# Kernel optimization log

Measured on AMD Instinct MI355X. Metric: run time of the kernel, lower is better.

## Reference

```python
import jax, jax.numpy as jnp
import numpy as np

N_NODES = 50000
N_EDGES = 800000
IN_DIM = 128
OUT_DIM = 128
N_HEADS = 4
HEAD_DIM = OUT_DIM // N_HEADS
EDGE_EMBED_DIM = 16
LN_EPS = 1e-5


def setup_inputs() -> dict:
    key = jax.random.key(0)
    ks = jax.random.split(key, 10)
    x = jax.random.normal(ks[0], (N_NODES, IN_DIM), dtype=jnp.float32)
    edge_index = jax.random.randint(ks[1], (2, N_EDGES), 0, N_NODES, dtype=jnp.int32)
    edge_type = jax.random.randint(ks[2], (N_EDGES,), 0, 3, dtype=jnp.int32)
    # parameters (xavier-ish scaling)
    W = jax.random.normal(ks[3], (OUT_DIM, IN_DIM), dtype=jnp.float32) * (1.0 / np.sqrt(IN_DIM))
    a_src = jax.random.normal(ks[4], (N_HEADS, HEAD_DIM), dtype=jnp.float32) * (1.0 / np.sqrt(HEAD_DIM))
    a_dst = jax.random.normal(ks[5], (N_HEADS, HEAD_DIM), dtype=jnp.float32) * (1.0 / np.sqrt(HEAD_DIM))
    a_edge = jax.random.normal(ks[6], (N_HEADS, EDGE_EMBED_DIM), dtype=jnp.float32) * (1.0 / np.sqrt(EDGE_EMBED_DIM))
    edge_embed = jax.random.normal(ks[7], (3, EDGE_EMBED_DIM), dtype=jnp.float32)
    ln_gamma = jnp.ones((OUT_DIM,), dtype=jnp.float32)
    ln_beta = jnp.zeros((OUT_DIM,), dtype=jnp.float32)
    return {"x": x, "edge_index": edge_index, "edge_type": edge_type,
            "W": W, "a_src": a_src, "a_dst": a_dst, "a_edge": a_edge,
            "edge_embed": edge_embed, "ln_gamma": ln_gamma, "ln_beta": ln_beta}


def reference(x, edge_index, edge_type, W, a_src, a_dst, a_edge, edge_embed, ln_gamma, ln_beta):
    N = x.shape[0]
    h = x @ W.T                                   # [N, out_dim]
    hh = h.reshape(N, N_HEADS, HEAD_DIM)          # [N, H, D]
    src, dst = edge_index[0], edge_index[1]       # [E]

    # per-node attention projections, then gather (avoids gathering full [E,H,D] twice)
    alpha_src = jnp.einsum('nhd,hd->nh', hh, a_src)   # [N, H]
    alpha_dst = jnp.einsum('nhd,hd->nh', hh, a_dst)   # [N, H]
    e_score = edge_embed[edge_type] @ a_edge.T        # [E, H]

    attn = alpha_src[src] + alpha_dst[dst] + e_score  # [E, H]
    attn = jax.nn.leaky_relu(attn, negative_slope=0.2)

    # segment softmax over incoming edges of each dst node
    attn_max = jax.ops.segment_max(attn, dst, num_segments=N)    # [N, H]
    attn_max = jnp.maximum(attn_max, -1e9)                       # match torch init fill
    attn_exp = jnp.exp(attn - attn_max[dst])                     # [E, H]
    attn_sum = jax.ops.segment_sum(attn_exp, dst, num_segments=N)
    attn_norm = attn_exp / (attn_sum[dst] + 1e-10)               # [E, H]

    # weighted scatter-aggregation (dropout is identity in eval)
    weighted = hh[src] * attn_norm[:, :, None]                   # [E, H, D]
    out = jax.ops.segment_sum(weighted, dst, num_segments=N)     # [N, H, D]
    out = out.reshape(N, OUT_DIM) + h                            # residual

    # LayerNorm over last dim
    mu = jnp.mean(out, axis=-1, keepdims=True)
    var = jnp.var(out, axis=-1, keepdims=True)
    out = (out - mu) * jax.lax.rsqrt(var + LN_EPS)
    return out * ln_gamma + ln_beta
```

## Files before the change

### kernel.cpp

```cpp
#include <hip/hip_runtime.h>

#define N_NODES 50000
#define N_EDGES 800000
#define IN_DIM 128
#define OUT_DIM 128
#define N_HEADS 4
#define HEAD_DIM 32
#define LN_EPS 1e-5f

#define WS_HB    0
#define WS_ASRC  3200000
#define WS_ADST  3400000
#define WS_ETAB  3600000
#define WS_DEG   3600016
#define WS_AVTAB 3650016
#define WS_OFFS  3650528
#define WS_PARTS 3700528
#define WS_EPACK 3700592
#define WS_RANK  4500608

#define SCAN_BLOCKS 49

typedef __bf16 bf16x8 __attribute__((ext_vector_type(8)));
typedef float  f32x4  __attribute__((ext_vector_type(4)));

__device__ __forceinline__ unsigned short f2bf(float f) {
    unsigned int u = __float_as_uint(f);
    u += 0x7FFF + ((u >> 16) & 1);
    return (unsigned short)(u >> 16);
}
#define BFLO(u) __uint_as_float((unsigned int)(u) << 16)
#define BFHI(u) __uint_as_float((unsigned int)(u) & 0xFFFF0000u)
#define LRELU(c) ((c) > 0.f ? (c) : 0.2f * (c))

__global__ __launch_bounds__(256) void zero_kernel(int4* __restrict__ p)
{
    int i = blockIdx.x * 256 + threadIdx.x;
    if (i < N_NODES / 4) p[i] = make_int4(0, 0, 0, 0);
}

__global__ __launch_bounds__(256) void count_prep_kernel(
    const int* __restrict__ dsts, int* __restrict__ deg, int* __restrict__ rank,
    const float* __restrict__ W, const float* __restrict__ a_src,
    const float* __restrict__ a_dst, const float* __restrict__ edge_embed,
    const float* __restrict__ a_edge, float* __restrict__ etab,
    unsigned short* __restrict__ avtab)
{
    int gid = blockIdx.x * 256 + threadIdx.x;
    if (gid < 12) {
        int t = gid >> 2, hh = gid & 3;
        float s = 0.f;
        for (int k = 0; k < 16; ++k) s += edge_embed[t * 16 + k] * a_edge[hh * 16 + k];
        etab[t * 4 + hh] = s;
    }
    if (gid < 1024) {
        int c8 = gid & 7, k = gid >> 3;
        int hh = c8 & 3;
        const float* av = (c8 < 4) ? a_src : a_dst;
        float s = 0.f;
        #pragma unroll 8
        for (int dd = 0; dd < 32; ++dd)
            s += W[(hh * 32 + dd) * 128 + k] * av[hh * 32 + dd];
        int kblk = k >> 5, g = (k & 31) >> 3, j = k & 7;
        avtab[((kblk * 64) + g * 16 + c8) * 8 + j] = f2bf(s);
    }
    if (gid < N_EDGES) rank[gid] = atomicAdd(&deg[dsts[gid]], 1);
}

__global__ __launch_bounds__(256) void gemm_mfma_kernel(
    const float* __restrict__ x, const float* __restrict__ W,
    const unsigned short* __restrict__ avtab,
    unsigned short* __restrict__ hb,
    float* __restrict__ alpha_src, float* __restrict__ alpha_dst)
{
    __shared__ bf16x8 wlds[2048];
    int tid = threadIdx.x;
    for (int f = tid; f < 2048; f += 256) {
        int ct = f >> 8, kb = (f >> 6) & 3, ln = f & 63;
        int d = ct * 16 + (ln & 15);
        int kbase = kb * 32 + ((ln >> 4) << 3);
        const float* wp = W + d * 128 + kbase;
        float4 w0 = *(const float4*)wp;
        float4 w1 = *(const float4*)(wp + 4);
        bf16x8 v;
        v[0] = (__bf16)w0.x; v[1] = (__bf16)w0.y; v[2] = (__bf16)w0.z; v[3] = (__bf16)w0.w;
        v[4] = (__bf16)w1.x; v[5] = (__bf16)w1.y; v[6] = (__bf16)w1.z; v[7] = (__bf16)w1.w;
        wlds[f] = v;
    }
    int lane = tid & 63, wid = tid >> 6;
    bf16x8 avf[4];
    const bf16x8* avp = (const bf16x8*)avtab;
    #pragma unroll
    for (int kb = 0; kb < 4; ++kb) avf[kb] = avp[kb * 64 + lane];
    __syncthreads();

    int r = lane & 15, g = lane >> 4;
    int tile = blockIdx.x * 4 + wid;
    if (tile >= N_NODES / 16) return;
    {
        const float* xp = x + ((size_t)tile * 16 + r) * 128 + g * 8;
        bf16x8 af[4];
        #pragma unroll
        for (int kb = 0; kb < 4; ++kb) {
            float4 x0 = *(const float4*)(xp + kb * 32);
            float4 x1 = *(const float4*)(xp + kb * 32 + 4);
            bf16x8 v;
            v[0] = (__bf16)x0.x; v[1] = (__bf16)x0.y; v[2] = (__bf16)x0.z; v[3] = (__bf16)x0.w;
            v[4] = (__bf16)x1.x; v[5] = (__bf16)x1.y; v[6] = (__bf16)x1.z; v[7] = (__bf16)x1.w;
            af[kb] = v;
        }
        f32x4 aacc = {0.f, 0.f, 0.f, 0.f};
        #pragma unroll
        for (int kb = 0; kb < 4; ++kb)
            aacc = __builtin_amdgcn_mfma_f32_16x16x32_bf16(af[kb], avf[kb], aacc, 0, 0, 0);

        int orow = tile * 16 + g * 4;
        #pragma unroll
        for (int ct = 0; ct < 8; ++ct) {
            f32x4 acc = {0.f, 0.f, 0.f, 0.f};
            #pragma unroll
            for (int kb = 0; kb < 4; ++kb)
                acc = __builtin_amdgcn_mfma_f32_16x16x32_bf16(af[kb], wlds[(ct * 4 + kb) * 64 + lane], acc, 0, 0, 0);
            #pragma unroll
            for (int q = 0; q < 4; ++q)
                hb[(size_t)(orow + q) * 128 + ct * 16 + r] = f2bf(acc[q]);
        }
        if (r < 8) {
            float* ap = (r < 4) ? (alpha_src + (r & 3)) : (alpha_dst + (r & 3));
            #pragma unroll
            for (int q = 0; q < 4; ++q)
                ap[(size_t)(orow + q) * 4] = aacc[q];
        }
    }
}

__global__ __launch_bounds__(1024) void scan_part_kernel(
    const int* __restrict__ deg, int* __restrict__ offs, int* __restrict__ parts)
{
    __shared__ int wsum[16];
    int i = blockIdx.x * 1024 + threadIdx.x;
    int lane = threadIdx.x & 63;
    int wid  = threadIdx.x >> 6;
    int v = (i < N_NODES) ? deg[i] : 0;
    int xinc = v;
    #pragma unroll
    for (int d = 1; d < 64; d <<= 1) {
        int y = __shfl_up(xinc, d);
        if (lane >= d) xinc += y;
    }
    if (lane == 63) wsum[wid] = xinc;
    __syncthreads();
    if (wid == 0) {
        int sv = (lane < 16) ? wsum[lane] : 0;
        #pragma unroll
        for (int d = 1; d < 16; d <<= 1) {
            int y = __shfl_up(sv, d);
            if (lane >= d) sv += y;
        }
        if (lane < 16) wsum[lane] = sv;
    }
    __syncthreads();
    int woff = (wid > 0) ? wsum[wid - 1] : 0;
    if (i < N_NODES) offs[i] = woff + xinc - v;
    if (threadIdx.x == 0) parts[blockIdx.x] = wsum[15];
}

__global__ __launch_bounds__(1024) void scan_add_kernel(
    int* __restrict__ offs, const int* __restrict__ parts)
{
    __shared__ int pre_s;
    if (threadIdx.x < 64) {
        int v = ((int)threadIdx.x < (int)blockIdx.x) ? parts[threadIdx.x] : 0;
        #pragma unroll
        for (int off = 32; off >= 1; off >>= 1) v += __shfl_xor(v, off);
        if (threadIdx.x == 0) pre_s = v;
    }
    __syncthreads();
    int i = blockIdx.x * 1024 + threadIdx.x;
    if (i < N_NODES) offs[i] += pre_s;
}

__global__ void fill_kernel(const int* __restrict__ srcs, const int* __restrict__ dsts,
                            const int* __restrict__ etype, const int* __restrict__ rank,
                            const int* __restrict__ offs, unsigned int* __restrict__ epack)
{
    int e = blockIdx.x * 256 + threadIdx.x;
    if (e < N_EDGES) {
        int d = dsts[e];
        int p = offs[d] + rank[e];
        epack[p] = (unsigned int)srcs[e] | ((unsigned int)etype[e] << 16);
    }
}

__global__ __launch_bounds__(256) void aggregate_kernel(
    const unsigned short* __restrict__ hb, const float* __restrict__ alpha_src,
    const float* __restrict__ alpha_dst, const float* __restrict__ etab,
    const unsigned int* __restrict__ epack, const int* __restrict__ offs,
    const float* __restrict__ gamma, const float* __restrict__ beta,
    float* __restrict__ out)
{
    int lane = threadIdx.x & 63;
    int wid  = threadIdx.x >> 6;
    int half = lane >> 5;
    int l5   = lane & 31;
    int n = blockIdx.x * 8 + wid * 2 + half;
    if (n >= N_NODES) return;

    int e0 = offs[n];
    int e1 = (n == N_NODES - 1) ? N_EDGES : offs[n + 1];
    int deg = e1 - e0;

    int g  = l5 >> 3;
    int sl = l5 & 7;
    int headL = sl >> 1;

    float ad_h = alpha_dst[(size_t)n * 4 + headL];
    float et0 = etab[0 * 4 + headL];
    float et1 = etab[1 * 4 + headL];
    float et2 = etab[2 * 4 + headL];

    float s = 0.f;
    float acc[16];
    #pragma unroll
    for (int k = 0; k < 16; ++k) acc[k] = 0.f;

    const unsigned int* ep = epack + e0;
    for (int j = g; j < deg; j += 4) {
        unsigned int p = ep[j];
        int si = p & 0xFFFF;
        int t  = p >> 16;
        float asv = alpha_src[(size_t)si * 4 + headL];
        const uint4* hp = (const uint4*)(hb + ((size_t)si << 7) + (sl << 4));
        uint4 hA = hp[0];
        uint4 hB = hp[1];
        float ev = (t == 0) ? et0 : ((t == 1) ? et1 : et2);
        float c = LRELU(asv + ad_h + ev);
        float w = __expf(c);
        s += w;
        acc[0]  += w * BFLO(hA.x); acc[1]  += w * BFHI(hA.x);
        acc[2]  += w * BFLO(hA.y); acc[3]  += w * BFHI(hA.y);
        acc[4]  += w * BFLO(hA.z); acc[5]  += w * BFHI(hA.z);
        acc[6]  += w * BFLO(hA.w); acc[7]  += w * BFHI(hA.w);
        acc[8]  += w * BFLO(hB.x); acc[9]  += w * BFHI(hB.x);
        acc[10] += w * BFLO(hB.y); acc[11] += w * BFHI(hB.y);
        acc[12] += w * BFLO(hB.z); acc[13] += w * BFHI(hB.z);
        acc[14] += w * BFLO(hB.w); acc[15] += w * BFHI(hB.w);
    }

    #pragma unroll
    for (int k = 0; k < 16; ++k) {
        acc[k] += __shfl_xor(acc[k], 8);
        acc[k] += __shfl_xor(acc[k], 16);
    }
    s += __shfl_xor(s, 8);
    s += __shfl_xor(s, 16);
    float rs = 1.0f / (s + 1e-10f);

    const uint4* rp = (const uint4*)(hb + ((size_t)n << 7) + (sl << 4));
    uint4 r0 = rp[0];
    uint4 r1 = rp[1];
    float o[16];
    o[0]  = acc[0]  * rs + BFLO(r0.x); o[1]  = acc[1]  * rs + BFHI(r0.x);
    o[2]  = acc[2]  * rs + BFLO(r0.y); o[3]  = acc[3]  * rs + BFHI(r0.y);
    o[4]  = acc[4]  * rs + BFLO(r0.z); o[5]  = acc[5]  * rs + BFHI(r0.z);
    o[6]  = acc[6]  * rs + BFLO(r0.w); o[7]  = acc[7]  * rs + BFHI(r0.w);
    o[8]  = acc[8]  * rs + BFLO(r1.x); o[9]  = acc[9]  * rs + BFHI(r1.x);
    o[10] = acc[10] * rs + BFLO(r1.y); o[11] = acc[11] * rs + BFHI(r1.y);
    o[12] = acc[12] * rs + BFLO(r1.z); o[13] = acc[13] * rs + BFHI(r1.z);
    o[14] = acc[14] * rs + BFLO(r1.w); o[15] = acc[15] * rs + BFHI(r1.w);

    float lsum = 0.f;
    #pragma unroll
    for (int k = 0; k < 16; ++k) lsum += o[k];
    #pragma unroll
    for (int off = 4; off >= 1; off >>= 1) lsum += __shfl_xor(lsum, off);
    float mean = lsum * (1.0f / 128.0f);
    float vs = 0.f;
    #pragma unroll
    for (int k = 0; k < 16; ++k) { float d = o[k] - mean; vs += d * d; }
    #pragma unroll
    for (int off = 4; off >= 1; off >>= 1) vs += __shfl_xor(vs, off);
    float inv = rsqrtf(vs * (1.0f / 128.0f) + LN_EPS);

    float4 gv = *(const float4*)(gamma + sl * 16 + g * 4);
    float4 bv = *(const float4*)(beta  + sl * 16 + g * 4);
    float4 wv;
    wv.x = (o[g * 4 + 0] - mean) * inv * gv.x + bv.x;
    wv.y = (o[g * 4 + 1] - mean) * inv * gv.y + bv.y;
    wv.z = (o[g * 4 + 2] - mean) * inv * gv.z + bv.z;
    wv.w = (o[g * 4 + 3] - mean) * inv * gv.w + bv.w;
    *(float4*)(out + (size_t)n * OUT_DIM + sl * 16 + g * 4) = wv;
}

extern "C" void kernel_launch(void* const* d_in, const int* in_sizes, int n_in,
                              void* d_out, int out_size, void* d_ws, size_t ws_size,
                              hipStream_t stream)
{
    const float* x          = (const float*)d_in[0];
    const int*   edge_index = (const int*)d_in[1];
    const int*   etype      = (const int*)d_in[2];
    const float* W          = (const float*)d_in[3];
    const float* a_src      = (const float*)d_in[4];
    const float* a_dst      = (const float*)d_in[5];
    const float* a_edge     = (const float*)d_in[6];
    const float* edge_embed = (const float*)d_in[7];
    const float* gamma      = (const float*)d_in[8];
    const float* beta       = (const float*)d_in[9];

    float* ws = (float*)d_ws;
    unsigned short* hb = (unsigned short*)(ws + WS_HB);
    float* asrc = ws + WS_ASRC;
    float* adst = ws + WS_ADST;
    float* etab = ws + WS_ETAB;
    int*   deg  = (int*)d_ws + WS_DEG;
    unsigned short* avtab = (unsigned short*)((int*)d_ws + WS_AVTAB);
    int*   offs = (int*)d_ws + WS_OFFS;
    int*   parts= (int*)d_ws + WS_PARTS;
    unsigned int* epack = (unsigned int*)d_ws + WS_EPACK;
    int*   rank = (int*)d_ws + WS_RANK;

    const int* srcs = edge_index;
    const int* dsts = edge_index + N_EDGES;

    zero_kernel<<<(N_NODES / 4 + 255) / 256, 256, 0, stream>>>((int4*)deg);
    count_prep_kernel<<<(N_EDGES + 255) / 256, 256, 0, stream>>>(
        dsts, deg, rank, W, a_src, a_dst, edge_embed, a_edge, etab, avtab);
    gemm_mfma_kernel<<<(N_NODES / 16 + 3) / 4, 256, 0, stream>>>(x, W, avtab, hb, asrc, adst);
    scan_part_kernel<<<SCAN_BLOCKS, 1024, 0, stream>>>(deg, offs, parts);
    scan_add_kernel<<<SCAN_BLOCKS, 1024, 0, stream>>>(offs, parts);
    fill_kernel<<<(N_EDGES + 255) / 256, 256, 0, stream>>>(srcs, dsts, etype, rank, offs, epack);
    aggregate_kernel<<<(N_NODES + 7) / 8, 256, 0, stream>>>(
        hb, asrc, adst, etab, epack, offs, gamma, beta, (float*)d_out);
}
```

Before: 118.9 us.

## Precompute per-edge attention weights in fill kernel; persistent-grid GEMM

Moves the attention logit and exp computation from the aggregate loop into the CSR fill kernel. Each edge's four per-head weights are written as a float4 in dst-sorted order, so aggregation now reads one contiguous weight instead of gathering alpha_src per edge and recomputing exp. The cost is an extra 12.8MB weight array that is written once and read back. Separately, the GEMM now runs on a fixed 512-block grid with a grid-stride loop over tiles.

After: 131.5 us. 10.6% more time.

```diff
diff --git a/kernel.cpp b/kernel.cpp
--- a/kernel.cpp
+++ b/kernel.cpp
@@ -18,6 +18,7 @@
 #define WS_PARTS 3700528
 #define WS_EPACK 3700592
 #define WS_RANK  4500608
+#define WS_WTS   5300608
 
 #define SCAN_BLOCKS 49
 
@@ -95,9 +96,7 @@
     __syncthreads();
 
     int r = lane & 15, g = lane >> 4;
-    int tile = blockIdx.x * 4 + wid;
-    if (tile >= N_NODES / 16) return;
-    {
+    for (int tile = blockIdx.x * 4 + wid; tile < N_NODES / 16; tile += gridDim.x * 4) {
         const float* xp = x + ((size_t)tile * 16 + r) * 128 + g * 8;
         bf16x8 af[4];
         #pragma unroll
@@ -182,20 +181,36 @@
 
 __global__ void fill_kernel(const int* __restrict__ srcs, const int* __restrict__ dsts,
                             const int* __restrict__ etype, const int* __restrict__ rank,
-                            const int* __restrict__ offs, unsigned int* __restrict__ epack)
+                            const int* __restrict__ offs,
+                            const float* __restrict__ alpha_src,
+                            const float* __restrict__ alpha_dst,
+                            const float* __restrict__ etab,
+                            unsigned int* __restrict__ epack,
+                            float4* __restrict__ wts)
 {
     int e = blockIdx.x * 256 + threadIdx.x;
     if (e < N_EDGES) {
         int d = dsts[e];
         int p = offs[d] + rank[e];
-        epack[p] = (unsigned int)srcs[e] | ((unsigned int)etype[e] << 16);
+        int src = srcs[e];
+        int t = etype[e];
+        float4 as = *(const float4*)(alpha_src + (size_t)src * 4);
+        float4 ad = *(const float4*)(alpha_dst + (size_t)d * 4);
+        float4 et = *(const float4*)(etab + t * 4);
+        float4 w;
+        w.x = __expf(LRELU(as.x + ad.x + et.x));
+        w.y = __expf(LRELU(as.y + ad.y + et.y));
+        w.z = __expf(LRELU(as.z + ad.z + et.z));
+        w.w = __expf(LRELU(as.w + ad.w + et.w));
+        epack[p] = (unsigned int)src;
+        wts[p] = w;
     }
 }
 
 __global__ __launch_bounds__(256) void aggregate_kernel(
-    const unsigned short* __restrict__ hb, const float* __restrict__ alpha_src,
-    const float* __restrict__ alpha_dst, const float* __restrict__ etab,
-    const unsigned int* __restrict__ epack, const int* __restrict__ offs,
+    const unsigned short* __restrict__ hb,
+    const unsigned int* __restrict__ epack, const float* __restrict__ wts,
+    const int* __restrict__ offs,
     const float* __restrict__ gamma, const float* __restrict__ beta,
     float* __restrict__ out)
 {
@@ -208,34 +223,25 @@
 
     int e0 = offs[n];
     int e1 = (n == N_NODES - 1) ? N_EDGES : offs[n + 1];
-    int deg = e1 - e0;
+    int dg = e1 - e0;
 
     int g  = l5 >> 3;
     int sl = l5 & 7;
     int headL = sl >> 1;
 
-    float ad_h = alpha_dst[(size_t)n * 4 + headL];
-    float et0 = etab[0 * 4 + headL];
-    float et1 = etab[1 * 4 + headL];
-    float et2 = etab[2 * 4 + headL];
-
     float s = 0.f;
     float acc[16];
     #pragma unroll
     for (int k = 0; k < 16; ++k) acc[k] = 0.f;
 
     const unsigned int* ep = epack + e0;
-    for (int j = g; j < deg; j += 4) {
-        unsigned int p = ep[j];
-        int si = p & 0xFFFF;
-        int t  = p >> 16;
-        float asv = alpha_src[(size_t)si * 4 + headL];
+    const float* wp = wts + (size_t)e0 * 4 + headL;
+    for (int j = g; j < dg; j += 4) {
+        unsigned int si = ep[j];
+        float w = wp[j * 4];
         const uint4* hp = (const uint4*)(hb + ((size_t)si << 7) + (sl << 4));
         uint4 hA = hp[0];
         uint4 hB = hp[1];
-        float ev = (t == 0) ? et0 : ((t == 1) ? et1 : et2);
-        float c = LRELU(asv + ad_h + ev);
-        float w = __expf(c);
         s += w;
         acc[0]  += w * BFLO(hA.x); acc[1]  += w * BFHI(hA.x);
         acc[2]  += w * BFLO(hA.y); acc[3]  += w * BFHI(hA.y);
@@ -318,6 +324,7 @@
     int*   parts= (int*)d_ws + WS_PARTS;
     unsigned int* epack = (unsigned int*)d_ws + WS_EPACK;
     int*   rank = (int*)d_ws + WS_RANK;
+    float* wts  = ws + WS_WTS;
 
     const int* srcs = edge_index;
     const int* dsts = edge_index + N_EDGES;
@@ -325,10 +332,11 @@
     zero_kernel<<<(N_NODES / 4 + 255) / 256, 256, 0, stream>>>((int4*)deg);
     count_prep_kernel<<<(N_EDGES + 255) / 256, 256, 0, stream>>>(
         dsts, deg, rank, W, a_src, a_dst, edge_embed, a_edge, etab, avtab);
-    gemm_mfma_kernel<<<(N_NODES / 16 + 3) / 4, 256, 0, stream>>>(x, W, avtab, hb, asrc, adst);
+    gemm_mfma_kernel<<<512, 256, 0, stream>>>(x, W, avtab, hb, asrc, adst);
     scan_part_kernel<<<SCAN_BLOCKS, 1024, 0, stream>>>(deg, offs, parts);
     scan_add_kernel<<<SCAN_BLOCKS, 1024, 0, stream>>>(offs, parts);
-    fill_kernel<<<(N_EDGES + 255) / 256, 256, 0, stream>>>(srcs, dsts, etype, rank, offs, epack);
+    fill_kernel<<<(N_EDGES + 255) / 256, 256, 0, stream>>>(
+        srcs, dsts, etype, rank, offs, asrc, adst, etab, epack, (float4*)wts);
     aggregate_kernel<<<(N_NODES + 7) / 8, 256, 0, stream>>>(
-        hb, asrc, adst, etab, epack, offs, gamma, beta, (float*)d_out);
-}
+        hb, epack, wts, offs, gamma, beta, (float*)d_out);
+}
```

## Cooperatively gather edge weights per half-wave and loop GEMM tiles persistently

Applied to the files above, without the earlier changes.

The aggregation kernel now has 32 lanes load up to 32 edge records at once and compute all four head weights per edge. It then broadcasts source index and bf16-packed weights by shuffle, while every lane gathers a 4-element slice of each neighbour row. This replaces the old scheme of 4 edge groups × 8 lanes each reading 16 elements, followed by a cross-group reduction. Attention weights are rounded to bf16 before accumulation, which adds precision loss. The early return for n >= N_NODES was removed, but 50000 divides evenly by 8 so it stays safe. The GEMM becomes a grid-stride loop over tiles with a fixed 512-block grid.

Result: slower. 123.9 us (+4.2%).

```diff
diff --git a/kernel.cpp b/kernel.cpp
--- a/kernel.cpp
+++ b/kernel.cpp
@@ -95,9 +95,7 @@
     __syncthreads();
 
     int r = lane & 15, g = lane >> 4;
-    int tile = blockIdx.x * 4 + wid;
-    if (tile >= N_NODES / 16) return;
-    {
+    for (int tile = blockIdx.x * 4 + wid; tile < N_NODES / 16; tile += gridDim.x * 4) {
         const float* xp = x + ((size_t)tile * 16 + r) * 128 + g * 8;
         bf16x8 af[4];
         #pragma unroll
@@ -204,92 +202,87 @@
     int half = lane >> 5;
     int l5   = lane & 31;
     int n = blockIdx.x * 8 + wid * 2 + half;
-    if (n >= N_NODES) return;
 
     int e0 = offs[n];
     int e1 = (n == N_NODES - 1) ? N_EDGES : offs[n + 1];
-    int deg = e1 - e0;
-
-    int g  = l5 >> 3;
-    int sl = l5 & 7;
-    int headL = sl >> 1;
-
-    float ad_h = alpha_dst[(size_t)n * 4 + headL];
-    float et0 = etab[0 * 4 + headL];
-    float et1 = etab[1 * 4 + headL];
-    float et2 = etab[2 * 4 + headL];
-
-    float s = 0.f;
-    float acc[16];
-    #pragma unroll
-    for (int k = 0; k < 16; ++k) acc[k] = 0.f;
+    int dg = e1 - e0;
+
+    int headL = l5 >> 3;
+
+    float4 adv = *(const float4*)(alpha_dst + (size_t)n * 4);
+    const float4* etabv = (const float4*)etab;
+
+    float4 s4 = make_float4(0.f, 0.f, 0.f, 0.f);
+    float acc0 = 0.f, acc1 = 0.f, acc2 = 0.f, acc3 = 0.f;
 
     const unsigned int* ep = epack + e0;
-    for (int j = g; j < deg; j += 4) {
-        unsigned int p = ep[j];
-        int si = p & 0xFFFF;
-        int t  = p >> 16;
-        float asv = alpha_src[(size_t)si * 4 + headL];
-        const uint4* hp = (const uint4*)(hb + ((size_t)si << 7) + (sl << 4));
-        uint4 hA = hp[0];
-        uint4 hB = hp[1];
-        float ev = (t == 0) ? et0 : ((t == 1) ? et1 : et2);
-        float c = LRELU(asv + ad_h + ev);
-        float w = __expf(c);
-        s += w;
-        acc[0]  += w * BFLO(hA.x); acc[1]  += w * BFHI(hA.x);
-        acc[2]  += w * BFLO(hA.y); acc[3]  += w * BFHI(hA.y);
-        acc[4]  += w * BFLO(hA.z); acc[5]  += w * BFHI(hA.z);
-        acc[6]  += w * BFLO(hA.w); acc[7]  += w * BFHI(hA.w);
-        acc[8]  += w * BFLO(hB.x); acc[9]  += w * BFHI(hB.x);
-        acc[10] += w * BFLO(hB.y); acc[11] += w * BFHI(hB.y);
-        acc[12] += w * BFLO(hB.z); acc[13] += w * BFHI(hB.z);
-        acc[14] += w * BFLO(hB.w); acc[15] += w * BFHI(hB.w);
-    }
-
-    #pragma unroll
-    for (int k = 0; k < 16; ++k) {
-        acc[k] += __shfl_xor(acc[k], 8);
-        acc[k] += __shfl_xor(acc[k], 16);
-    }
-    s += __shfl_xor(s, 8);
-    s += __shfl_xor(s, 16);
+    int nb = (dg + 31) >> 5;
+    for (int b = 0; b < nb; ++b) {
+        int jb = b << 5;
+        int myj = jb + l5;
+        bool valid = myj < dg;
+        unsigned int p = 0;
+        if (valid) p = ep[myj];
+        int sim = p & 0xFFFF;
+        int t   = p >> 16;
+        float4 al = *(const float4*)(alpha_src + (size_t)sim * 4);
+        float4 et = etabv[t];
+        float w0 = valid ? __expf(LRELU(al.x + adv.x + et.x)) : 0.f;
+        float w1 = valid ? __expf(LRELU(al.y + adv.y + et.y)) : 0.f;
+        float w2 = valid ? __expf(LRELU(al.z + adv.z + et.z)) : 0.f;
+        float w3 = valid ? __expf(LRELU(al.w + adv.w + et.w)) : 0.f;
+        s4.x += w0; s4.y += w1; s4.z += w2; s4.w += w3;
+        int up0 = (int)(((unsigned)f2bf(w1) << 16) | f2bf(w0));
+        int up1 = (int)(((unsigned)f2bf(w3) << 16) | f2bf(w2));
+
+        int cnt = (dg - jb < 32) ? (dg - jb) : 32;
+        #pragma unroll 4
+        for (int j = 0; j < cnt; ++j) {
+            int sj = __shfl(sim, j, 32);
+            int u0 = __shfl(up0, j, 32);
+            int u1 = __shfl(up1, j, 32);
+            unsigned int pick = (unsigned int)((headL & 2) ? u1 : u0);
+            float w = (headL & 1) ? BFHI(pick) : BFLO(pick);
+            uint2 hv = *(const uint2*)(hb + ((size_t)sj << 7) + (l5 << 2));
+            acc0 += w * BFLO(hv.x); acc1 += w * BFHI(hv.x);
+            acc2 += w * BFLO(hv.y); acc3 += w * BFHI(hv.y);
+        }
+    }
+
+    #pragma unroll
+    for (int off = 16; off >= 1; off >>= 1) {
+        s4.x += __shfl_xor(s4.x, off);
+        s4.y += __shfl_xor(s4.y, off);
+        s4.z += __shfl_xor(s4.z, off);
+        s4.w += __shfl_xor(s4.w, off);
+    }
+    float s = (headL & 2) ? ((headL & 1) ? s4.w : s4.z) : ((headL & 1) ? s4.y : s4.x);
     float rs = 1.0f / (s + 1e-10f);
 
-    const uint4* rp = (const uint4*)(hb + ((size_t)n << 7) + (sl << 4));
-    uint4 r0 = rp[0];
-    uint4 r1 = rp[1];
-    float o[16];
-    o[0]  = acc[0]  * rs + BFLO(r0.x); o[1]  = acc[1]  * rs + BFHI(r0.x);
-    o[2]  = acc[2]  * rs + BFLO(r0.y); o[3]  = acc[3]  * rs + BFHI(r0.y);
-    o[4]  = acc[4]  * rs + BFLO(r0.z); o[5]  = acc[5]  * rs + BFHI(r0.z);
-    o[6]  = acc[6]  * rs + BFLO(r0.w); o[7]  = acc[7]  * rs + BFHI(r0.w);
-    o[8]  = acc[8]  * rs + BFLO(r1.x); o[9]  = acc[9]  * rs + BFHI(r1.x);
-    o[10] = acc[10] * rs + BFLO(r1.y); o[11] = acc[11] * rs + BFHI(r1.y);
-    o[12] = acc[12] * rs + BFLO(r1.z); o[13] = acc[13] * rs + BFHI(r1.z);
-    o[14] = acc[14] * rs + BFLO(r1.w); o[15] = acc[15] * rs + BFHI(r1.w);
-
-    float lsum = 0.f;
-    #pragma unroll
-    for (int k = 0; k < 16; ++k) lsum += o[k];
-    #pragma unroll
-    for (int off = 4; off >= 1; off >>= 1) lsum += __shfl_xor(lsum, off);
+    uint2 rv = *(const uint2*)(hb + ((size_t)n << 7) + (l5 << 2));
+    float o0 = acc0 * rs + BFLO(rv.x);
+    float o1 = acc1 * rs + BFHI(rv.x);
+    float o2 = acc2 * rs + BFLO(rv.y);
+    float o3 = acc3 * rs + BFHI(rv.y);
+
+    float lsum = o0 + o1 + o2 + o3;
+    #pragma unroll
+    for (int off = 16; off >= 1; off >>= 1) lsum += __shfl_xor(lsum, off);
     float mean = lsum * (1.0f / 128.0f);
-    float vs = 0.f;
-    #pragma unroll
-    for (int k = 0; k < 16; ++k) { float d = o[k] - mean; vs += d * d; }
-    #pragma unroll
-    for (int off = 4; off >= 1; off >>= 1) vs += __shfl_xor(vs, off);
+    float d0 = o0 - mean, d1 = o1 - mean, d2 = o2 - mean, d3 = o3 - mean;
+    float vs = d0 * d0 + d1 * d1 + d2 * d2 + d3 * d3;
+    #pragma unroll
+    for (int off = 16; off >= 1; off >>= 1) vs += __shfl_xor(vs, off);
     float inv = rsqrtf(vs * (1.0f / 128.0f) + LN_EPS);
 
-    float4 gv = *(const float4*)(gamma + sl * 16 + g * 4);
-    float4 bv = *(const float4*)(beta  + sl * 16 + g * 4);
+    float4 gv = *(const float4*)(gamma + l5 * 4);
+    float4 bv = *(const float4*)(beta  + l5 * 4);
     float4 wv;
-    wv.x = (o[g * 4 + 0] - mean) * inv * gv.x + bv.x;
-    wv.y = (o[g * 4 + 1] - mean) * inv * gv.y + bv.y;
-    wv.z = (o[g * 4 + 2] - mean) * inv * gv.z + bv.z;
-    wv.w = (o[g * 4 + 3] - mean) * inv * gv.w + bv.w;
-    *(float4*)(out + (size_t)n * OUT_DIM + sl * 16 + g * 4) = wv;
+    wv.x = d0 * inv * gv.x + bv.x;
+    wv.y = d1 * inv * gv.y + bv.y;
+    wv.z = d2 * inv * gv.z + bv.z;
+    wv.w = d3 * inv * gv.w + bv.w;
+    *(float4*)(out + (size_t)n * OUT_DIM + l5 * 4) = wv;
 }
 
 extern "C" void kernel_launch(void* const* d_in, const int* in_sizes, int n_in,
@@ -325,7 +318,7 @@
     zero_kernel<<<(N_NODES / 4 + 255) / 256, 256, 0, stream>>>((int4*)deg);
     count_prep_kernel<<<(N_EDGES + 255) / 256, 256, 0, stream>>>(
         dsts, deg, rank, W, a_src, a_dst, edge_embed, a_edge, etab, avtab);
-    gemm_mfma_kernel<<<(N_NODES / 16 + 3) / 4, 256, 0, stream>>>(x, W, avtab, hb, asrc, adst);
+    gemm_mfma_kernel<<<512, 256, 0, stream>>>(x, W, avtab, hb, asrc, adst);
     scan_part_kernel<<<SCAN_BLOCKS, 1024, 0, stream>>>(deg, offs, parts);
     scan_add_kernel<<<SCAN_BLOCKS, 1024, 0, stream>>>(offs, parts);
     fill_kernel<<<(N_EDGES + 255) / 256, 256, 0, stream>>>(srcs, dsts, etype, rank, offs, epack);
```
